# Kernel optimization log

Hardware: AMD Instinct MI355X
Metric: run time of the kernel (lower is better)

## Reference

```python
import jax, jax.numpy as jnp
import numpy as np

NUM_HEADS = 12
HIDDEN = 768
HEAD_DIM = HIDDEN // NUM_HEADS  # 64
B, S = 2, 2048


def setup_inputs() -> dict:
    key = jax.random.key(0)
    ks = jax.random.split(key, 8)
    inp = {
        "hidden_states": jax.random.normal(ks[0], (B, S, HIDDEN), dtype=jnp.float32),
        "attention_mask": jnp.zeros((B, 1, 1, S), dtype=jnp.float32),
        "Wq": jax.random.normal(ks[1], (HIDDEN, HIDDEN), dtype=jnp.float32) * 0.02,
        "bq": jnp.zeros((HIDDEN,), dtype=jnp.float32),
        "Wk": jax.random.normal(ks[2], (HIDDEN, HIDDEN), dtype=jnp.float32) * 0.02,
        "bk": jnp.zeros((HIDDEN,), dtype=jnp.float32),
        "Wv": jax.random.normal(ks[3], (HIDDEN, HIDDEN), dtype=jnp.float32) * 0.02,
        "bv": jnp.zeros((HIDDEN,), dtype=jnp.float32),
    }
    return inp


def _split_heads(x):
    # [B, S, H*d] -> [B, H, S, d]
    b, s, _ = x.shape
    return x.reshape(b, s, NUM_HEADS, HEAD_DIM).transpose(0, 2, 1, 3)


def reference(hidden_states, attention_mask, Wq, bq, Wk, bk, Wv, bv):
    # Q/K/V projections (nn.Linear: x @ W.T + b; W generated square so direct matmul is equivalent math)
    q = _split_heads(hidden_states @ Wq + bq)  # [B,H,S,d]
    k = _split_heads(hidden_states @ Wk + bk)
    v = _split_heads(hidden_states @ Wv + bv)

    scale = 1.0 / np.sqrt(HEAD_DIM).astype(np.float32)
    scores = jnp.einsum("bhqd,bhkd->bhqk", q, k) * scale  # [B,H,S,S]
    scores = scores + attention_mask  # additive mask, broadcast [B,1,1,S]
    probs = jax.nn.softmax(scores, axis=-1)
    # dropout prob = 0.0 -> identity (eval mode)
    ctx = jnp.einsum("bhqk,bhkd->bhqd", probs, v)  # [B,H,S,d]
    ctx = ctx.transpose(0, 2, 1, 3).reshape(hidden_states.shape[0], hidden_states.shape[1], HIDDEN)
    return ctx
```

## Files before the change

kernel.cpp:

```cpp
#include <hip/hip_runtime.h>

#define S_LEN 2048
#define HID   768
#define NH    12
#define HD    64
#define BATCH 2
#define GK    768
#define L2E   1.44269504088896340736f
#define QSCL  (0.125f * L2E)

typedef __attribute__((ext_vector_type(8))) short bf16x8;
typedef __attribute__((ext_vector_type(4))) float f32x4;
typedef __attribute__((ext_vector_type(4))) short s16x4;
typedef __attribute__((ext_vector_type(8))) short s16x8;

__device__ __forceinline__ unsigned short f2bf(float f) {
    union { float f; unsigned int u; } v; v.f = f;
    unsigned int r = v.u + 0x7fffu + ((v.u >> 16) & 1u);
    return (unsigned short)(r >> 16);
}
__device__ __forceinline__ unsigned short f2bf_hu(float f) {
    union { float f; unsigned int u; } v; v.f = f;
    return (unsigned short)((v.u + 0x8000u) >> 16);
}

#define GLL16(gp, lp) __builtin_amdgcn_global_load_lds( \
    (const __attribute__((address_space(1))) unsigned int*)(gp), \
    (__attribute__((address_space(3))) unsigned int*)(lp), 16, 0, 0)


__global__ __launch_bounds__(256) void prep_kernel(
    const float* __restrict__ X, const float* __restrict__ Wq,
    const float* __restrict__ Wk, const float* __restrict__ Wv,
    unsigned short* __restrict__ Xb, unsigned short* __restrict__ Wt) {
    __shared__ float T[32][33];
    int bid = blockIdx.x;
    if (bid < 3072) {
        int id = bid * 256 + threadIdx.x;
        float4 v = ((const float4*)X)[id];
        s16x4 o; o[0] = (short)f2bf(v.x); o[1] = (short)f2bf(v.y);
        o[2] = (short)f2bf(v.z); o[3] = (short)f2bf(v.w);
        ((s16x4*)Xb)[id] = o;
        return;
    }
    int t2 = bid - 3072;
    int mat = t2 / 576, t = t2 % 576;
    int tk = t / 24, tn = t % 24;
    const float* W = (mat == 0) ? Wq : (mat == 1) ? Wk : Wv;
    const float scl = (mat == 0) ? QSCL : 1.0f;
    int r  = threadIdx.x >> 3;
    int c4 = (threadIdx.x & 7) * 4;
    float4 v = *(const float4*)&W[(size_t)(tk*32 + r) * GK + tn*32 + c4];
    T[c4+0][r] = v.x; T[c4+1][r] = v.y; T[c4+2][r] = v.z; T[c4+3][r] = v.w;
    __syncthreads();
    s16x4 o;
    o[0] = (short)f2bf(T[r][c4+0] * scl); o[1] = (short)f2bf(T[r][c4+1] * scl);
    o[2] = (short)f2bf(T[r][c4+2] * scl); o[3] = (short)f2bf(T[r][c4+3] * scl);
    *(s16x4*)&Wt[(size_t)(mat*768 + tn*32 + r) * GK + tk*32 + c4] = o;
}

__global__ __launch_bounds__(256) void gemm_qkv(
    const unsigned short* __restrict__ Xb, const unsigned short* __restrict__ Wt,
    const float* __restrict__ bq, const float* __restrict__ bk,
    const float* __restrict__ bv,
    unsigned short* __restrict__ qb, unsigned short* __restrict__ kb,
    unsigned short* __restrict__ vb) {
    __shared__ __align__(16) unsigned short As[128][64];
    __shared__ __align__(16) unsigned short Bs[64][64];

    const int tid = threadIdx.x;
    const int bm = blockIdx.y * 128;
    const int bn = blockIdx.x * 64;
    const int w = tid >> 6, l = tid & 63, quad = l >> 4, lq = l & 15;
    const int wx = w & 1, wy = w >> 1;

    const int srow = l >> 3, schunk = ((l & 7) ^ (l >> 3)) * 8;
    const unsigned short* aga = Xb + (size_t)(bm + w*32 + srow) * GK + schunk;
    const unsigned short* bga = Wt + (size_t)(bn + w*16 + srow) * GK + schunk;

    const int c0 = ((quad)     ^ (lq & 7)) * 8;
    const int c1 = ((4 + quad) ^ (lq & 7)) * 8;

    f32x4 zero = {0.f, 0.f, 0.f, 0.f};
    f32x4 acc[4][2];
#pragma unroll
    for (int mi = 0; mi < 4; mi++)
#pragma unroll
        for (int ni = 0; ni < 2; ni++) acc[mi][ni] = zero;

    for (int k0 = 0; k0 < GK; k0 += 64) {
        __syncthreads();
#pragma unroll
        for (int i = 0; i < 4; i++)
            GLL16(aga + k0 + i*8*GK, &As[w*32 + i*8][0]);
#pragma unroll
        for (int i = 0; i < 2; i++)
            GLL16(bga + k0 + i*8*GK, &Bs[w*16 + i*8][0]);
        __syncthreads();
#pragma unroll
        for (int kh = 0; kh < 2; kh++) {
            const int cc = kh ? c1 : c0;
            bf16x8 a[4], b[2];
#pragma unroll
            for (int mi = 0; mi < 4; mi++)
                a[mi] = *(const bf16x8*)&As[wy*64 + mi*16 + lq][cc];
#pragma unroll
            for (int ni = 0; ni < 2; ni++)
                b[ni] = *(const bf16x8*)&Bs[wx*32 + ni*16 + lq][cc];
#pragma unroll
            for (int mi = 0; mi < 4; mi++)
#pragma unroll
                for (int ni = 0; ni < 2; ni++)
                    acc[mi][ni] = __builtin_amdgcn_mfma_f32_16x16x32_bf16(
                        a[mi], b[ni], acc[mi][ni], 0, 0, 0);
        }
    }

    const int mat = bn / 768;
    const float* bias = (mat == 0) ? bq : (mat == 1) ? bk : bv;
    const float bscl = (mat == 0) ? QSCL : 1.0f;
    const int nbase = bn % 768;
#pragma unroll
    for (int ni = 0; ni < 2; ni++) {
        int hn = nbase + wx*32 + ni*16 + lq;
        float bval = bias[hn] * bscl;
        int h = hn >> 6, d = hn & 63;
#pragma unroll
        for (int mi = 0; mi < 4; mi++) {
            int m0 = bm + wy*64 + mi*16 + quad*4;
            int b_ = m0 >> 11, s0 = m0 & 2047;
            if (mat != 1) {
                unsigned short* outp = (mat == 0) ? qb : vb;
                s16x4 pk;
#pragma unroll
                for (int r = 0; r < 4; r++) pk[r] = (short)f2bf_hu(acc[mi][ni][r] + bval);
                *(s16x4*)&outp[((size_t)((b_*NH + h) * HD + d)) * S_LEN + s0] = pk;
            } else {
                size_t base = ((size_t)((b_*NH + h) * S_LEN + s0)) * HD + d;
#pragma unroll
                for (int r = 0; r < 4; r++)
                    kb[base + (size_t)r * HD] = f2bf_hu(acc[mi][ni][r] + bval);
            }
        }
    }
}

__global__ __launch_bounds__(256) void attn_kernel(
    const unsigned short* __restrict__ Qtg, const unsigned short* __restrict__ Kg,
    const unsigned short* __restrict__ Vtg, const float* __restrict__ maskg,
    float* __restrict__ out) {
    __shared__ __align__(16) unsigned short Ks[2][64][64];
    __shared__ __align__(16) unsigned short Vt[2][64][64];
    __shared__ __align__(16) unsigned short Ps[4][16][72];
    __shared__ __align__(16) float mkL[S_LEN];

    const int tid = threadIdx.x;
    const int w = tid >> 6, l = tid & 63, quad = l >> 4, lq = l & 15;
    const int bh = blockIdx.y;
    const int q0 = blockIdx.x * 64;
    const int bi = bh / NH, hi = bh % NH;
    const unsigned short* Kh = Kg + (size_t)bh * S_LEN * HD;
    const unsigned short* Vh = Vtg + (size_t)bh * HD * S_LEN;

    bf16x8 a0, a1;
    {
        const unsigned short* Qt = Qtg + (size_t)bh * HD * S_LEN + (q0 + w*16 + lq);
#pragma unroll
        for (int j = 0; j < 8; j++) {
            a0[j] = (short)Qt[(size_t)(quad*8 + j) * S_LEN];
            a1[j] = (short)Qt[(size_t)(quad*8 + j + 32) * S_LEN];
        }
    }

    {
        const float4* mb4 = (const float4*)(maskg + (size_t)bi * S_LEN);
#pragma unroll
        for (int i = 0; i < 2; i++) {
            int idx = i * 256 + tid;
            float4 v = mb4[idx];
            float4 sv; sv.x = v.x*L2E; sv.y = v.y*L2E; sv.z = v.z*L2E; sv.w = v.w*L2E;
            ((float4*)mkL)[idx] = sv;
        }
    }

    bf16x8 ones;
#pragma unroll
    for (int i = 0; i < 8; i++) ones[i] = (short)0x3F80;

    const int srow = l >> 3, schunk = ((l & 7) ^ (l >> 3)) * 8;
    const unsigned short* kga = Kh + (size_t)(w*16 + srow) * HD + schunk;
    const unsigned short* vga = Vh + (size_t)(w*16 + srow) * S_LEN + schunk;

    const int c0 = ((quad)     ^ (lq & 7)) * 8;
    const int c1 = ((4 + quad) ^ (lq & 7)) * 8;

    f32x4 zero = {0.f, 0.f, 0.f, 0.f};
    f32x4 o[4], lsum = zero;
#pragma unroll
    for (int ng = 0; ng < 4; ng++) o[ng] = zero;

    auto stage = [&](int buf, int kt) {
#pragma unroll
        for (int i = 0; i < 2; i++) {
            GLL16(kga + (size_t)kt*64*HD + i*8*HD, &Ks[buf][w*16 + i*8][0]);
            GLL16(vga + kt*64 + (size_t)i*8*S_LEN, &Vt[buf][w*16 + i*8][0]);
        }
    };

    auto compute = [&](int buf, int kt) {
        const int kk = kt * 64;
        float mm[4];
#pragma unroll
        for (int g = 0; g < 4; g++) mm[g] = mkL[kk + g*16 + lq];

        f32x4 s[4];
#pragma unroll
        for (int g = 0; g < 4; g++) {
            bf16x8 b0 = *(const bf16x8*)&Ks[buf][g*16 + lq][c0];
            bf16x8 b1 = *(const bf16x8*)&Ks[buf][g*16 + lq][c1];
            f32x4 z = __builtin_amdgcn_mfma_f32_16x16x32_bf16(a0, b0, zero, 0, 0, 0);
            s[g]    = __builtin_amdgcn_mfma_f32_16x16x32_bf16(a1, b1, z,    0, 0, 0);
        }

#pragma unroll
        for (int g = 0; g < 4; g++) {
            const int col = g*16 + lq;
#pragma unroll
            for (int r = 0; r < 4; r++)
                Ps[w][quad*4 + r][col] = f2bf_hu(exp2f(s[g][r] + mm[g]));
        }

        bf16x8 pa0 = *(const bf16x8*)&Ps[w][lq][quad*8];
        bf16x8 pa1 = *(const bf16x8*)&Ps[w][lq][32 + quad*8];

        lsum = __builtin_amdgcn_mfma_f32_16x16x32_bf16(pa0, ones, lsum, 0, 0, 0);
        lsum = __builtin_amdgcn_mfma_f32_16x16x32_bf16(pa1, ones, lsum, 0, 0, 0);

#pragma unroll
        for (int ng = 0; ng < 4; ng++) {
            bf16x8 v0 = *(const bf16x8*)&Vt[buf][ng*16 + lq][c0];
            bf16x8 v1 = *(const bf16x8*)&Vt[buf][ng*16 + lq][c1];
            f32x4 t = __builtin_amdgcn_mfma_f32_16x16x32_bf16(pa0, v0, o[ng], 0, 0, 0);
            o[ng]   = __builtin_amdgcn_mfma_f32_16x16x32_bf16(pa1, v1, t,     0, 0, 0);
        }
    };

    stage(0, 0);
    __syncthreads();

    for (int kt = 0; kt < S_LEN / 64; kt += 2) {
        stage(1, kt + 1);
        compute(0, kt);
        __syncthreads();
        if (kt + 2 < S_LEN / 64) stage(0, kt + 2);
        compute(1, kt + 1);
        __syncthreads();
    }

#pragma unroll
    for (int r = 0; r < 4; r++) {
        const float inv = 1.0f / lsum[r];
        const int row = q0 + w*16 + quad*4 + r;
#pragma unroll
        for (int ng = 0; ng < 4; ng++)
            out[((size_t)(bi * S_LEN + row)) * HID + hi*HD + ng*16 + lq] = o[ng][r] * inv;
    }
}

extern "C" void kernel_launch(void* const* d_in, const int* in_sizes, int n_in,
                              void* d_out, int out_size, void* d_ws, size_t ws_size,
                              hipStream_t stream) {
    const float* X    = (const float*)d_in[0];
    const float* mask = (const float*)d_in[1];
    const float* Wq   = (const float*)d_in[2];
    const float* bq   = (const float*)d_in[3];
    const float* Wk   = (const float*)d_in[4];
    const float* bk   = (const float*)d_in[5];
    const float* Wv   = (const float*)d_in[6];
    const float* bv   = (const float*)d_in[7];
    float* out = (float*)d_out;

    const size_t per = (size_t)BATCH * NH * S_LEN * HD;
    unsigned short* qb = (unsigned short*)d_ws;
    unsigned short* kb = qb + per;
    unsigned short* vb = kb + per;
    unsigned short* xb = vb + per;
    unsigned short* wt = xb + (size_t)4096 * GK;

    prep_kernel<<<4800, 256, 0, stream>>>(X, Wq, Wk, Wv, xb, wt);

    dim3 ggrid(2304 / 64, 4096 / 128);
    gemm_qkv<<<ggrid, 256, 0, stream>>>(xb, wt, bq, bk, bv, qb, kb, vb);

    dim3 agrid(S_LEN / 64, BATCH * NH);
    attn_kernel<<<agrid, 256, 0, stream>>>(qb, kb, vb, mask, out);
}
```

Before: 162.5 us.

## Transpose score MFMA, pack P with cvt_pk, swizzle P LDS, remap workgroups

```diff
diff --git a/kernel.cpp b/kernel.cpp
--- a/kernel.cpp
+++ b/kernel.cpp
@@ -22,6 +22,12 @@
 __device__ __forceinline__ unsigned short f2bf_hu(float f) {
     union { float f; unsigned int u; } v; v.f = f;
     return (unsigned short)((v.u + 0x8000u) >> 16);
+}
+
+__device__ __forceinline__ unsigned int cvtpk(float a, float b) {
+    unsigned int r;
+    asm("v_cvt_pk_bf16_f32 %0, %1, %2" : "=v"(r) : "v"(a), "v"(b));
+    return r;
 }
 
 #define GLL16(gp, lp) __builtin_amdgcn_global_load_lds( \
@@ -151,13 +157,16 @@
     float* __restrict__ out) {
     __shared__ __align__(16) unsigned short Ks[2][64][64];
     __shared__ __align__(16) unsigned short Vt[2][64][64];
-    __shared__ __align__(16) unsigned short Ps[4][16][72];
+    __shared__ __align__(16) unsigned short Ps[4][16][64];
     __shared__ __align__(16) float mkL[S_LEN];
 
     const int tid = threadIdx.x;
     const int w = tid >> 6, l = tid & 63, quad = l >> 4, lq = l & 15;
-    const int bh = blockIdx.y;
-    const int q0 = blockIdx.x * 64;
+
+    const int wgid = blockIdx.y * gridDim.x + blockIdx.x;
+    const int virt = (wgid & 7) * 96 + (wgid >> 3);
+    const int bh = virt >> 5;
+    const int q0 = (virt & 31) * 64;
     const int bi = bh / NH, hi = bh % NH;
     const unsigned short* Kh = Kg + (size_t)bh * S_LEN * HD;
     const unsigned short* Vh = Vtg + (size_t)bh * HD * S_LEN;
@@ -193,6 +202,9 @@
 
     const int c0 = ((quad)     ^ (lq & 7)) * 8;
     const int c1 = ((4 + quad) ^ (lq & 7)) * 8;
+    const int pqh = quad >> 1;
+    const int po  = (quad & 1) * 4;
+    const int pe  = lq & 7;
 
     f32x4 zero = {0.f, 0.f, 0.f, 0.f};
     f32x4 o[4], lsum = zero;
@@ -209,29 +221,31 @@
 
     auto compute = [&](int buf, int kt) {
         const int kk = kt * 64;
-        float mm[4];
-#pragma unroll
-        for (int g = 0; g < 4; g++) mm[g] = mkL[kk + g*16 + lq];
-
-        f32x4 s[4];
+
+        f32x4 st[4];
 #pragma unroll
         for (int g = 0; g < 4; g++) {
             bf16x8 b0 = *(const bf16x8*)&Ks[buf][g*16 + lq][c0];
             bf16x8 b1 = *(const bf16x8*)&Ks[buf][g*16 + lq][c1];
-            f32x4 z = __builtin_amdgcn_mfma_f32_16x16x32_bf16(a0, b0, zero, 0, 0, 0);
-            s[g]    = __builtin_amdgcn_mfma_f32_16x16x32_bf16(a1, b1, z,    0, 0, 0);
+            f32x4 z = __builtin_amdgcn_mfma_f32_16x16x32_bf16(b0, a0, zero, 0, 0, 0);
+            st[g]   = __builtin_amdgcn_mfma_f32_16x16x32_bf16(b1, a1, z,    0, 0, 0);
         }
 
 #pragma unroll
         for (int g = 0; g < 4; g++) {
-            const int col = g*16 + lq;
-#pragma unroll
-            for (int r = 0; r < 4; r++)
-                Ps[w][quad*4 + r][col] = f2bf_hu(exp2f(s[g][r] + mm[g]));
-        }
-
-        bf16x8 pa0 = *(const bf16x8*)&Ps[w][lq][quad*8];
-        bf16x8 pa1 = *(const bf16x8*)&Ps[w][lq][32 + quad*8];
+            const f32x4 mmg = *(const f32x4*)&mkL[kk + g*16 + quad*4];
+            float p0 = exp2f(st[g][0] + mmg[0]);
+            float p1 = exp2f(st[g][1] + mmg[1]);
+            float p2 = exp2f(st[g][2] + mmg[2]);
+            float p3 = exp2f(st[g][3] + mmg[3]);
+            uint2 pr;
+            pr.x = cvtpk(p0, p1);
+            pr.y = cvtpk(p2, p3);
+            *(uint2*)&Ps[w][lq][((g*2 + pqh) ^ pe) * 8 + po] = pr;
+        }
+
+        bf16x8 pa0 = *(const bf16x8*)&Ps[w][lq][c0];
+        bf16x8 pa1 = *(const bf16x8*)&Ps[w][lq][c1];
 
         lsum = __builtin_amdgcn_mfma_f32_16x16x32_bf16(pa0, ones, lsum, 0, 0, 0);
         lsum = __builtin_amdgcn_mfma_f32_16x16x32_bf16(pa1, ones, lsum, 0, 0, 0);
```

New measurement: 160.3 us. About the same (-1.4%).
